# Kernel optimization log

Hardware: AMD Instinct MI355X
Metric: run time of the kernel (lower is better)

## Reference

```python
import jax, jax.numpy as jnp
import numpy as np

RATIO = 0.5  # SAGPooling ratio


def setup_inputs() -> dict:
    key = jax.random.key(0)
    ks = jax.random.split(key, 6)
    B, n, d, out_dim, Eg = 128, 512, 256, 256, 4096  # graphs, nodes/graph, feat, proj out, edges/graph
    N = B * n
    x = jax.random.normal(ks[0], (N, d), dtype=jnp.float32)
    # edges connect nodes within the same graph (contiguous node blocks)
    src = jax.random.randint(ks[1], (B, Eg), 0, n)
    dst = jax.random.randint(ks[2], (B, Eg), 0, n)
    off = (jnp.arange(B) * n)[:, None]
    edge_index = jnp.stack([(src + off).reshape(-1), (dst + off).reshape(-1)]).astype(jnp.int32)
    batch = jnp.repeat(jnp.arange(B), n).astype(jnp.int32)
    s = 1.0 / np.sqrt(d).astype(np.float32)
    w_rel = jax.random.normal(ks[3], (d, 1), dtype=jnp.float32) * s   # GraphConv lin_rel (has bias)
    b_rel = jnp.zeros((1,), dtype=jnp.float32)
    w_root = jax.random.normal(ks[4], (d, 1), dtype=jnp.float32) * s  # GraphConv lin_root (no bias)
    w_proj = jax.random.normal(ks[5], (d, out_dim), dtype=jnp.float32) * s  # projection Linear
    b_proj = jnp.zeros((out_dim,), dtype=jnp.float32)
    return {"x": x, "edge_index": edge_index, "batch": batch, "num_graphs": B,
            "w_rel": w_rel, "b_rel": b_rel, "w_root": w_root,
            "w_proj": w_proj, "b_proj": b_proj}


def reference(x, edge_index, batch, num_graphs, w_rel, b_rel, w_root, w_proj, b_proj):
    N, d = x.shape
    n = N // num_graphs                    # equal-size graphs
    k = int(np.ceil(RATIO * n))            # PyG topk: ceil(ratio * num_nodes)
    src, dst = edge_index[0], edge_index[1]
    # GraphConv(node_dim, 1): score_i = lin_rel(sum_{j->i} x_j) + lin_root(x_i)
    agg = jax.ops.segment_sum(x[src], dst, num_segments=N)          # [N, d]
    score = jnp.tanh((agg @ w_rel + b_rel + x @ w_root)[:, 0])       # [N], tanh nonlinearity
    sb = score.reshape(num_graphs, n)                                # [B, n]
    top_vals, top_idx = jax.lax.top_k(sb, k)                         # per-graph topk
    xb = x.reshape(num_graphs, n, d)
    x_sel = jnp.take_along_axis(xb, top_idx[:, :, None], axis=1)     # [B, k, d]
    x_sel = x_sel * top_vals[:, :, None]                             # x[perm] * score[perm] (multiplier=1)
    pooled = x_sel.mean(axis=1)                                      # global_mean_pool over k kept nodes
    return pooled @ w_proj + b_proj                                  # [B, out_dim]
```

## Files before the change

### kernel.cpp

```cpp
#include <hip/hip_runtime.h>

#define D        256
#define NPG      512
#define BG       128
#define KSEL     256
#define EPG      4096
#define NN       (BG * NPG)
#define ET       (BG * EPG)

__global__ __launch_bounds__(1024) void k_mega(
        const float* __restrict__ x, const int* __restrict__ ei,
        const float* __restrict__ w_rel, const float* __restrict__ b_rel,
        const float* __restrict__ w_root,
        const float* __restrict__ w_proj, const float* __restrict__ b_proj,
        float* __restrict__ out) {
    __shared__ __align__(16) float s_p[NPG];
    __shared__ __align__(16) float s_r[NPG];
    __shared__ __align__(16) float s_agg[NPG];
    __shared__ __align__(16) float s_val[NPG];
    __shared__ int   s_cnt2[1024];
    __shared__ int   s_selid[KSEL];
    __shared__ __align__(16) float s_selv[KSEL];
    __shared__ __align__(16) float s_pool[D];
    __shared__ __align__(16) float s_red[16][D];
    __shared__ int   s_nsel;

    int b = blockIdx.x, tid = threadIdx.x;
    int wave = tid >> 6, lane = tid & 63;
    int base = b * NPG;

    if (tid < NPG) s_agg[tid] = 0.f;
    if (tid == 0)  s_nsel = 0;

    {
        int sub = tid & 15;
        int nid = tid >> 4;
        float4 wr[4], wo[4];
        #pragma unroll
        for (int i = 0; i < 4; ++i) {
            wr[i] = ((const float4*)w_rel)[i * 16 + sub];
            wo[i] = ((const float4*)w_root)[i * 16 + sub];
        }
        #pragma unroll
        for (int pass = 0; pass < 8; ++pass) {
            int node = pass * 64 + nid;
            const float4* xr = (const float4*)(x + (size_t)(base + node) * D);
            float pv = 0.f, rv = 0.f;
            #pragma unroll
            for (int i = 0; i < 4; ++i) {
                float4 xv = xr[i * 16 + sub];
                pv += xv.x * wr[i].x + xv.y * wr[i].y + xv.z * wr[i].z + xv.w * wr[i].w;
                rv += xv.x * wo[i].x + xv.y * wo[i].y + xv.z * wo[i].z + xv.w * wo[i].w;
            }
            #pragma unroll
            for (int off = 8; off; off >>= 1) {
                pv += __shfl_xor(pv, off, 64);
                rv += __shfl_xor(rv, off, 64);
            }
            if (sub == 0) { s_p[node] = pv; s_r[node] = rv; }
        }
    }
    __syncthreads();

    {
        const int* src = ei + (size_t)b * EPG;
        const int* dst = ei + ET + (size_t)b * EPG;
        #pragma unroll
        for (int e = tid; e < EPG; e += 1024)
            atomicAdd(&s_agg[dst[e] - base], s_p[src[e] - base]);
    }
    __syncthreads();

    if (tid < NPG)
        s_val[tid] = tanhf(s_agg[tid] + b_rel[0] + s_r[tid]);
    __syncthreads();

    {
        int j = tid & (NPG - 1);
        int half = tid >> 9;
        float sv = s_val[j];
        int lo = half * (NPG / 2);
        const float4* v4 = (const float4*)(s_val + lo);
        int c = 0;
        #pragma unroll 8
        for (int q = 0; q < NPG / 8; ++q) {
            float4 o = v4[q];
            int i0 = lo + q * 4;
            c += (o.x > sv) || (o.x == sv && (i0 + 0) < j);
            c += (o.y > sv) || (o.y == sv && (i0 + 1) < j);
            c += (o.z > sv) || (o.z == sv && (i0 + 2) < j);
            c += (o.w > sv) || (o.w == sv && (i0 + 3) < j);
        }
        s_cnt2[tid] = c;
    }
    __syncthreads();
    if (tid < NPG) {
        int rank = s_cnt2[tid] + s_cnt2[tid + NPG];
        if (rank < KSEL) {
            int pos = atomicAdd(&s_nsel, 1);
            s_selid[pos] = tid;
            s_selv[pos]  = s_val[tid];
        }
    }
    __syncthreads();

    {
        float4 acc = {0.f, 0.f, 0.f, 0.f};
        #pragma unroll
        for (int m = 0; m < 16; ++m) {
            int s   = wave * 16 + m;
            int row = s_selid[s];
            float v = s_selv[s];
            float4 xv = ((const float4*)(x + (size_t)(base + row) * D))[lane];
            acc.x += v * xv.x; acc.y += v * xv.y;
            acc.z += v * xv.z; acc.w += v * xv.w;
        }
        ((float4*)s_red[wave])[lane] = acc;
    }
    __syncthreads();
    if (tid < D) {
        float s = 0.f;
        #pragma unroll
        for (int w = 0; w < 16; ++w) s += s_red[w][tid];
        s_pool[tid] = s;
    }
    __syncthreads();

    {
        int f = tid & (D - 1);
        int q = tid >> 8;
        const float4* pool4 = (const float4*)s_pool + q * 16;
        const float* wp = w_proj + (size_t)(q * 64) * D + f;
        float acc = 0.f;
        #pragma unroll
        for (int t = 0; t < 16; ++t) {
            float4 pv = pool4[t];
            acc += pv.x * wp[(t * 4 + 0) * D];
            acc += pv.y * wp[(t * 4 + 1) * D];
            acc += pv.z * wp[(t * 4 + 2) * D];
            acc += pv.w * wp[(t * 4 + 3) * D];
        }
        s_red[q][f] = acc;
    }
    __syncthreads();
    if (tid < D)
        out[(size_t)b * D + tid] = b_proj[tid] +
            (s_red[0][tid] + s_red[1][tid] + s_red[2][tid] + s_red[3][tid]) * (1.0f / KSEL);
}

extern "C" void kernel_launch(void* const* d_in, const int* in_sizes, int n_in,
                              void* d_out, int out_size, void* d_ws, size_t ws_size,
                              hipStream_t stream) {
    const float* x      = (const float*)d_in[0];
    const int*   ei     = (const int*)d_in[1];
    const float* w_rel  = (const float*)d_in[4];
    const float* b_rel  = (const float*)d_in[5];
    const float* w_root = (const float*)d_in[6];
    const float* w_proj = (const float*)d_in[7];
    const float* b_proj = (const float*)d_in[8];
    float* out = (float*)d_out;

    k_mega<<<BG, 1024, 0, stream>>>(x, ei, w_rel, b_rel, w_root, w_proj, b_proj, out);
}
```

Before: 135.7 us.

## Split per-node score projection into a separate fully parallel kernel

Measured after the change: 135.6 us. No clear change (-0.1%).

```diff
diff --git a/kernel.cpp b/kernel.cpp
--- a/kernel.cpp
+++ b/kernel.cpp
@@ -8,14 +8,35 @@
 #define NN       (BG * NPG)
 #define ET       (BG * EPG)
 
-__global__ __launch_bounds__(1024) void k_mega(
+__global__ __launch_bounds__(256) void k_proj_scores(
+        const float* __restrict__ x,
+        const float* __restrict__ w_rel, const float* __restrict__ w_root,
+        float* __restrict__ p, float* __restrict__ r) {
+    int tid  = threadIdx.x;
+    int wave = tid >> 6, lane = tid & 63;
+    int node = blockIdx.x * 4 + wave;
+
+    const float4* x4  = (const float4*)(x + (size_t)node * D);
+    float4 xv = x4[lane];
+    float4 wr = ((const float4*)w_rel)[lane];
+    float4 wo = ((const float4*)w_root)[lane];
+    float pv = xv.x * wr.x + xv.y * wr.y + xv.z * wr.z + xv.w * wr.w;
+    float rv = xv.x * wo.x + xv.y * wo.y + xv.z * wo.z + xv.w * wo.w;
+    #pragma unroll
+    for (int off = 32; off; off >>= 1) {
+        pv += __shfl_xor(pv, off, 64);
+        rv += __shfl_xor(rv, off, 64);
+    }
+    if (lane == 0) { p[node] = pv; r[node] = rv; }
+}
+
+__global__ __launch_bounds__(1024) void k_select_pool(
         const float* __restrict__ x, const int* __restrict__ ei,
-        const float* __restrict__ w_rel, const float* __restrict__ b_rel,
-        const float* __restrict__ w_root,
+        const float* __restrict__ p, const float* __restrict__ r,
+        const float* __restrict__ b_rel,
         const float* __restrict__ w_proj, const float* __restrict__ b_proj,
         float* __restrict__ out) {
     __shared__ __align__(16) float s_p[NPG];
-    __shared__ __align__(16) float s_r[NPG];
     __shared__ __align__(16) float s_agg[NPG];
     __shared__ __align__(16) float s_val[NPG];
     __shared__ int   s_cnt2[1024];
@@ -29,37 +50,8 @@
     int wave = tid >> 6, lane = tid & 63;
     int base = b * NPG;
 
-    if (tid < NPG) s_agg[tid] = 0.f;
+    if (tid < NPG) { s_p[tid] = p[base + tid]; s_agg[tid] = 0.f; }
     if (tid == 0)  s_nsel = 0;
-
-    {
-        int sub = tid & 15;
-        int nid = tid >> 4;
-        float4 wr[4], wo[4];
-        #pragma unroll
-        for (int i = 0; i < 4; ++i) {
-            wr[i] = ((const float4*)w_rel)[i * 16 + sub];
-            wo[i] = ((const float4*)w_root)[i * 16 + sub];
-        }
-        #pragma unroll
-        for (int pass = 0; pass < 8; ++pass) {
-            int node = pass * 64 + nid;
-            const float4* xr = (const float4*)(x + (size_t)(base + node) * D);
-            float pv = 0.f, rv = 0.f;
-            #pragma unroll
-            for (int i = 0; i < 4; ++i) {
-                float4 xv = xr[i * 16 + sub];
-                pv += xv.x * wr[i].x + xv.y * wr[i].y + xv.z * wr[i].z + xv.w * wr[i].w;
-                rv += xv.x * wo[i].x + xv.y * wo[i].y + xv.z * wo[i].z + xv.w * wo[i].w;
-            }
-            #pragma unroll
-            for (int off = 8; off; off >>= 1) {
-                pv += __shfl_xor(pv, off, 64);
-                rv += __shfl_xor(rv, off, 64);
-            }
-            if (sub == 0) { s_p[node] = pv; s_r[node] = rv; }
-        }
-    }
     __syncthreads();
 
     {
@@ -72,7 +64,7 @@
     __syncthreads();
 
     if (tid < NPG)
-        s_val[tid] = tanhf(s_agg[tid] + b_rel[0] + s_r[tid]);
+        s_val[tid] = tanhf(s_agg[tid] + b_rel[0] + r[base + tid]);
     __syncthreads();
 
     {
@@ -160,5 +152,9 @@
     const float* b_proj = (const float*)d_in[8];
     float* out = (float*)d_out;
 
-    k_mega<<<BG, 1024, 0, stream>>>(x, ei, w_rel, b_rel, w_root, w_proj, b_proj, out);
+    float* p = (float*)d_ws;
+    float* r = p + NN;
+
+    k_proj_scores<<<NN / 4, 256, 0, stream>>>(x, w_rel, w_root, p, r);
+    k_select_pool<<<BG, 1024, 0, stream>>>(x, ei, p, r, b_rel, w_proj, b_proj, out);
 }
```
